# Performance work log

Hardware: AMD Instinct MI355X
Metric: run time of the kernel (lower is better)

Reference implementation:

```python
import jax, jax.numpy as jnp
import numpy as np

B, IN, HID, EMB, K = 65536, 256, 256, 64, 4096
EPS = 1e-5  # BatchNorm1d default eps


def setup_inputs() -> dict:
    key = jax.random.key(0)
    ks = jax.random.split(key, 12)
    s = 0.05
    return {
        "x": jax.random.normal(ks[0], (B, IN), jnp.float32),
        "W1": jax.random.normal(ks[1], (HID, IN), jnp.float32) * s,
        "b1": jax.random.normal(ks[2], (HID,), jnp.float32) * s,
        "gamma": jnp.ones((HID,), jnp.float32),
        "beta": jnp.zeros((HID,), jnp.float32),
        "mean": jax.random.normal(ks[3], (HID,), jnp.float32) * s,
        "var": jax.random.uniform(ks[4], (HID,), jnp.float32, 0.5, 1.5),
        "W2": jax.random.normal(ks[5], (HID // 2, HID), jnp.float32) * s,
        "b2": jax.random.normal(ks[6], (HID // 2,), jnp.float32) * s,
        "W3": jax.random.normal(ks[7], (EMB, HID // 2), jnp.float32) * s,
        "b3": jax.random.normal(ks[8], (EMB,), jnp.float32) * s,
        "codebook": jax.random.normal(ks[9], (K, EMB), jnp.float32),
    }


def reference(x, W1, b1, gamma, beta, mean, var, W2, b2, W3, b3, codebook):
    # encoder: Linear -> BatchNorm1d (eval stats) -> ReLU -> Linear -> ReLU -> Linear -> Tanh
    h = x @ W1.T + b1                                   # [B, HID]
    h = (h - mean) * jax.lax.rsqrt(var + EPS) * gamma + beta
    h = jax.nn.relu(h)
    h = jax.nn.relu(h @ W2.T + b2)                      # [B, HID//2]
    z = jnp.tanh(h @ W3.T + b3)                         # [B, EMB]
    # squared-distance matrix: ||z||^2 + ||e||^2 - 2 z e^T  -> [B, K]
    d = (jnp.sum(z * z, axis=1, keepdims=True)
         + jnp.sum(codebook * codebook, axis=1)
         - 2.0 * (z @ codebook.T))
    return jnp.argmin(d, axis=1)                        # [B] int token indices
```

## Files before the change

### kernel.cpp

```cpp
#include <hip/hip_runtime.h>

#define IN_DIM  256
#define HID_DIM 256
#define H2_DIM  128
#define EMB_DIM 64
#define K_CODES 4096
#define EPS_BN  1e-5f


typedef _Float16 f16;
typedef _Float16 f16x4 __attribute__((ext_vector_type(4)));
typedef _Float16 f16x8 __attribute__((ext_vector_type(8)));
typedef float    f32x16 __attribute__((ext_vector_type(16)));

__global__ __launch_bounds__(256) void k_norms(const float* __restrict__ cb,
                                               float* __restrict__ norms) {
    int c = blockIdx.x * 256 + threadIdx.x;
    const float4* row = reinterpret_cast<const float4*>(cb + (size_t)c * EMB_DIM);
    float s = 0.f;
#pragma unroll
    for (int i = 0; i < EMB_DIM / 4; ++i) {
        float4 v = row[i];
        s += v.x * v.x + v.y * v.y + v.z * v.z + v.w * v.w;
    }
    norms[c] = 0.5f * s;
}

__global__ __launch_bounds__(256) void k_prep(
    const float* __restrict__ W1, const float* __restrict__ W2,
    const float* __restrict__ W3, const float* __restrict__ cb,
    f16* __restrict__ p1h, f16* __restrict__ p1l,
    f16* __restrict__ p2h, f16* __restrict__ p2l,
    f16* __restrict__ p3h, f16* __restrict__ p3l,
    f16* __restrict__ cfh, f16* __restrict__ cfl) {
    int t = blockIdx.x * 256 + threadIdx.x;
    const float* src; f16 *dh, *dl; int tt, row, k0, K;
    if (t < 8192) {
        tt = t; int f = tt >> 6, l = tt & 63;
        int ct = f & 7, kst = f >> 3;
        row = ct * 32 + (l & 31); k0 = kst * 16 + (l >> 5) * 8;
        src = W1; K = IN_DIM; dh = p1h; dl = p1l;
    } else if (t < 12288) {
        tt = t - 8192; int f = tt >> 6, l = tt & 63;
        int ct = f & 3, kst = f >> 2;
        row = ct * 32 + (l & 31); k0 = kst * 16 + (l >> 5) * 8;
        src = W2; K = HID_DIM; dh = p2h; dl = p2l;
    } else if (t < 13312) {
        tt = t - 12288; int f = tt >> 6, l = tt & 63;
        int ct = f & 1, ks = f >> 1;
        row = ct * 32 + (l & 31); k0 = ks * 16 + (l >> 5) * 8;
        src = W3; K = H2_DIM; dh = p3h; dl = p3l;
    } else {
        tt = t - 13312; int f = tt >> 6, l = tt & 63;
        int ct = f & 3, ks = (f >> 2) & 3, ch = f >> 4;
        row = ch * 128 + ct * 32 + (l & 31); k0 = ks * 16 + (l >> 5) * 8;
        src = cb; K = EMB_DIM; dh = cfh; dl = cfl;
    }
    const float* s = src + (size_t)row * K + k0;
    f16x8 hv, lv;
#pragma unroll
    for (int j = 0; j < 8; ++j) {
        float v = s[j];
        f16 h = (f16)v;
        hv[j] = h;
        lv[j] = (f16)(v - (float)h);
    }
    *(f16x8*)(dh + (size_t)tt * 8) = hv;
    *(f16x8*)(dl + (size_t)tt * 8) = lv;
}

__global__ __launch_bounds__(256) void k_encoder_mfma(
    const float* __restrict__ x,
    const f16* __restrict__ p1h, const f16* __restrict__ p1l,
    const f16* __restrict__ p2h, const f16* __restrict__ p2l,
    const f16* __restrict__ p3h, const f16* __restrict__ p3l,
    const float* __restrict__ b1,
    const float* __restrict__ gm, const float* __restrict__ bt,
    const float* __restrict__ mu, const float* __restrict__ vr,
    const float* __restrict__ b2, const float* __restrict__ b3,
    f16* __restrict__ Zh, f16* __restrict__ Zl) {
    __shared__ __align__(16) f16 sm[25600];
    const int tid  = threadIdx.x;
    const int lane = tid & 63;
    const int w    = tid >> 6;
    const int ln31 = lane & 31;
    const int q    = lane >> 5;
    const int r0   = blockIdx.x * 32;

#pragma unroll
    for (int it = 0; it < 8; ++it) {
        int i = it * 256 + tid;
        int row = i >> 6, c4 = (i & 63) * 4;
        float4 v = *reinterpret_cast<const float4*>(
            x + (size_t)(r0 + row) * IN_DIM + c4);
        f16x4 hv, lv;
        hv[0] = (f16)v.x; lv[0] = (f16)(v.x - (float)hv[0]);
        hv[1] = (f16)v.y; lv[1] = (f16)(v.y - (float)hv[1]);
        hv[2] = (f16)v.z; lv[2] = (f16)(v.z - (float)hv[2]);
        hv[3] = (f16)v.w; lv[3] = (f16)(v.w - (float)hv[3]);
        *(f16x4*)(sm + row * 264 + c4)        = hv;
        *(f16x4*)(sm + 8448 + row * 264 + c4) = lv;
    }
    __syncthreads();

    f32x16 acc1a = {};
    f32x16 acc1b = {};
    {
        const f16* q1h = p1h + (size_t)(2 * w) * 512 + lane * 8;
        const f16* q1l = p1l + (size_t)(2 * w) * 512 + lane * 8;
        f16x8 bh0 = *(const f16x8*)(q1h);
        f16x8 bh1 = *(const f16x8*)(q1h + 512);
        f16x8 bl0 = *(const f16x8*)(q1l);
        f16x8 bl1 = *(const f16x8*)(q1l + 512);
#pragma unroll 2
        for (int kst = 0; kst < 16; ++kst) {
            f16x8 ch0 = bh0, ch1 = bh1, cl0 = bl0, cl1 = bl1;
            int kn = (kst + 1) & 15;
            bh0 = *(const f16x8*)(q1h + (size_t)kn * 4096);
            bh1 = *(const f16x8*)(q1h + (size_t)kn * 4096 + 512);
            bl0 = *(const f16x8*)(q1l + (size_t)kn * 4096);
            bl1 = *(const f16x8*)(q1l + (size_t)kn * 4096 + 512);
            int koff = kst * 16 + q * 8;
            f16x8 ah = *(const f16x8*)(sm + ln31 * 264 + koff);
            f16x8 al = *(const f16x8*)(sm + 8448 + ln31 * 264 + koff);
            acc1a = __builtin_amdgcn_mfma_f32_32x32x16_f16(ah, ch0, acc1a, 0, 0, 0);
            acc1b = __builtin_amdgcn_mfma_f32_32x32x16_f16(ah, ch1, acc1b, 0, 0, 0);
            acc1a = __builtin_amdgcn_mfma_f32_32x32x16_f16(al, ch0, acc1a, 0, 0, 0);
            acc1b = __builtin_amdgcn_mfma_f32_32x32x16_f16(al, ch1, acc1b, 0, 0, 0);
            acc1a = __builtin_amdgcn_mfma_f32_32x32x16_f16(ah, cl0, acc1a, 0, 0, 0);
            acc1b = __builtin_amdgcn_mfma_f32_32x32x16_f16(ah, cl1, acc1b, 0, 0, 0);
        }
    }
    __syncthreads();

    {
#pragma unroll
        for (int nt = 0; nt < 2; ++nt) {
            int j = w * 64 + nt * 32 + ln31;
            float sc = gm[j] * rsqrtf(vr[j] + EPS_BN);
            float sh = (b1[j] - mu[j]) * sc + bt[j];
            const f32x16& a = nt ? acc1b : acc1a;
#pragma unroll
            for (int r = 0; r < 16; ++r) {
                int row = (r & 3) + 8 * (r >> 2) + 4 * q;
                float v = a[r] * sc + sh;
                v = v > 0.f ? v : 0.f;
                f16 h = (f16)v;
                sm[row * 264 + j]        = h;
                sm[8448 + row * 264 + j] = (f16)(v - (float)h);
            }
        }
    }
    __syncthreads();

    f32x16 acc2a = {};
    f32x16 acc2b = {};
    {
        const f16* q2h = p2h + (size_t)w * 512 + lane * 8;
        const f16* q2l = p2l + (size_t)w * 512 + lane * 8;
        f16x8 bh = *(const f16x8*)(q2h);
        f16x8 bl = *(const f16x8*)(q2l);
#pragma unroll 2
        for (int kst = 0; kst < 16; ++kst) {
            f16x8 cbh = bh, cbl = bl;
            int kn = (kst + 1) & 15;
            bh = *(const f16x8*)(q2h + (size_t)kn * 2048);
            bl = *(const f16x8*)(q2l + (size_t)kn * 2048);
            int koff = kst * 16 + q * 8;
            f16x8 ah = *(const f16x8*)(sm + ln31 * 264 + koff);
            f16x8 al = *(const f16x8*)(sm + 8448 + ln31 * 264 + koff);
            f32x16& acc = (kst & 1) ? acc2b : acc2a;
            acc = __builtin_amdgcn_mfma_f32_32x32x16_f16(ah, cbh, acc, 0, 0, 0);
            acc = __builtin_amdgcn_mfma_f32_32x32x16_f16(al, cbh, acc, 0, 0, 0);
            acc = __builtin_amdgcn_mfma_f32_32x32x16_f16(ah, cbl, acc, 0, 0, 0);
        }
    }
    {
        int j2 = w * 32 + ln31;
        float bias = b2[j2];
#pragma unroll
        for (int r = 0; r < 16; ++r) {
            int row = (r & 3) + 8 * (r >> 2) + 4 * q;
            float v = (acc2a[r] + acc2b[r]) + bias;
            v = v > 0.f ? v : 0.f;
            f16 h = (f16)v;
            sm[16896 + row * 136 + j2] = h;
            sm[21248 + row * 136 + j2] = (f16)(v - (float)h);
        }
    }
    __syncthreads();

    if (w < 2) {
        f32x16 acc3a = {};
        f32x16 acc3b = {};
        const f16* q3h = p3h + (size_t)w * 512 + lane * 8;
        const f16* q3l = p3l + (size_t)w * 512 + lane * 8;
        f16x8 bh = *(const f16x8*)(q3h);
        f16x8 bl = *(const f16x8*)(q3l);
#pragma unroll 2
        for (int ks = 0; ks < 8; ++ks) {
            f16x8 cbh = bh, cbl = bl;
            int kn = (ks + 1) & 7;
            bh = *(const f16x8*)(q3h + (size_t)kn * 1024);
            bl = *(const f16x8*)(q3l + (size_t)kn * 1024);
            f16x8 ah = *(const f16x8*)(sm + 16896 + ln31 * 136 + ks * 16 + q * 8);
            f16x8 al = *(const f16x8*)(sm + 21248 + ln31 * 136 + ks * 16 + q * 8);
            f32x16& acc = (ks & 1) ? acc3b : acc3a;
            acc = __builtin_amdgcn_mfma_f32_32x32x16_f16(ah, cbh, acc, 0, 0, 0);
            acc = __builtin_amdgcn_mfma_f32_32x32x16_f16(al, cbh, acc, 0, 0, 0);
            acc = __builtin_amdgcn_mfma_f32_32x32x16_f16(ah, cbl, acc, 0, 0, 0);
        }
        int j3 = w * 32 + ln31;
        float bias = b3[j3];
#pragma unroll
        for (int r = 0; r < 16; ++r) {
            int row = (r & 3) + 8 * (r >> 2) + 4 * q;
            float zv = tanhf((acc3a[r] + acc3b[r]) + bias);
            f16 h = (f16)zv;
            size_t idx = (size_t)(r0 + row) * EMB_DIM + j3;
            Zh[idx] = h;
            Zl[idx] = (f16)(zv - (float)h);
        }
    }
}

__global__ __launch_bounds__(512) void k_argmin_mfma(
    const f16* __restrict__ Zh, const f16* __restrict__ Zl,
    const f16* __restrict__ cfh, const f16* __restrict__ cfl,
    const float* __restrict__ norms, int* __restrict__ out) {
    __shared__ __align__(16) f16 sm[16896];
    const int tid  = threadIdx.x;
    const int lane = tid & 63;
    const int w    = tid >> 6;
    const int rt   = w & 3;
    const int hp   = w >> 2;
    const int ln31 = lane & 31;
    const int q    = lane >> 5;
    const int r0   = blockIdx.x * 128;

    f16x8 ah[4], al[4];
#pragma unroll
    for (int ks = 0; ks < 4; ++ks) {
        size_t zoff = (size_t)(r0 + rt * 32 + ln31) * EMB_DIM + ks * 16 + q * 8;
        ah[ks] = *(const f16x8*)(Zh + zoff);
        al[ks] = *(const f16x8*)(Zl + zoff);
    }

    float bv[16];
    int   bi[16];
#pragma unroll
    for (int i = 0; i < 16; ++i) { bv[i] = -3.4e38f; bi[i] = 0; }

#pragma unroll 1
    for (int s = 0; s < 64; ++s) {
        int ch = s >> 1;
        int ct = hp * 2 + (s & 1);
        size_t fb = (size_t)(ch * 16 + ct) * 512 + lane * 8;
        f16x8 bh[4], bl[4];
#pragma unroll
        for (int ks = 0; ks < 4; ++ks) {
            bh[ks] = *(const f16x8*)(cfh + fb + (size_t)ks * 2048);
            bl[ks] = *(const f16x8*)(cfl + fb + (size_t)ks * 2048);
        }
        f32x16 acc0 = {};
        f32x16 acc1 = {};
#pragma unroll
        for (int ks = 0; ks < 4; ks += 2) {
            acc0 = __builtin_amdgcn_mfma_f32_32x32x16_f16(ah[ks],     bh[ks],     acc0, 0, 0, 0);
            acc1 = __builtin_amdgcn_mfma_f32_32x32x16_f16(ah[ks + 1], bh[ks + 1], acc1, 0, 0, 0);
            acc0 = __builtin_amdgcn_mfma_f32_32x32x16_f16(al[ks],     bh[ks],     acc0, 0, 0, 0);
            acc1 = __builtin_amdgcn_mfma_f32_32x32x16_f16(al[ks + 1], bh[ks + 1], acc1, 0, 0, 0);
            acc0 = __builtin_amdgcn_mfma_f32_32x32x16_f16(ah[ks],     bl[ks],     acc0, 0, 0, 0);
            acc1 = __builtin_amdgcn_mfma_f32_32x32x16_f16(ah[ks + 1], bl[ks + 1], acc1, 0, 0, 0);
        }
        int   col = ch * 128 + ct * 32 + ln31;
        float nv  = norms[col];
#pragma unroll
        for (int r = 0; r < 16; ++r) {
            float t  = (acc0[r] + acc1[r]) - nv;
            bool  gt = t > bv[r];
            bv[r] = gt ? t : bv[r];
            bi[r] = gt ? col : bi[r];
        }
    }

    __syncthreads();
    {
        float* pv = (float*)sm;
        int*   pi = (int*)sm + 4096;
        if (w >= 4) {
#pragma unroll
            for (int r = 0; r < 16; ++r) {
                pv[(w - 4) * 1024 + lane * 16 + r] = bv[r];
                pi[(w - 4) * 1024 + lane * 16 + r] = bi[r];
            }
        }
        __syncthreads();
        if (w < 4) {
#pragma unroll
            for (int r = 0; r < 16; ++r) {
                float v2 = pv[w * 1024 + lane * 16 + r];
                int   i2 = pi[w * 1024 + lane * 16 + r];
                bool tk = (v2 > bv[r]) || (v2 == bv[r] && i2 < bi[r]);
                bv[r] = tk ? v2 : bv[r];
                bi[r] = tk ? i2 : bi[r];
            }
        }
    }
    __syncthreads();

    float* redv = (float*)sm;
    int*   redi = (int*)sm + 4224;
    if (w < 4) {
#pragma unroll
        for (int r = 0; r < 16; ++r) {
            int row = (r & 3) + 8 * (r >> 2) + 4 * q + 32 * w;
            redv[row * 33 + ln31] = bv[r];
            redi[row * 33 + ln31] = bi[r];
        }
    }
    __syncthreads();
    if (tid < 128) {
        float v  = redv[tid * 33];
        int   ix = redi[tid * 33];
#pragma unroll
        for (int j = 1; j < 32; ++j) {
            float vj = redv[tid * 33 + j];
            int   ij = redi[tid * 33 + j];
            if (vj > v || (vj == v && ij < ix)) { v = vj; ix = ij; }
        }
        out[r0 + tid] = ix;
    }
}

extern "C" void kernel_launch(void* const* d_in, const int* in_sizes, int n_in,
                              void* d_out, int out_size, void* d_ws, size_t ws_size,
                              hipStream_t stream) {
    (void)n_in; (void)out_size; (void)ws_size;
    const float* x  = (const float*)d_in[0];
    const float* W1 = (const float*)d_in[1];
    const float* b1 = (const float*)d_in[2];
    const float* gm = (const float*)d_in[3];
    const float* bt = (const float*)d_in[4];
    const float* mu = (const float*)d_in[5];
    const float* vr = (const float*)d_in[6];
    const float* W2 = (const float*)d_in[7];
    const float* b2 = (const float*)d_in[8];
    const float* W3 = (const float*)d_in[9];
    const float* b3 = (const float*)d_in[10];
    const float* cb = (const float*)d_in[11];

    char* ws = (char*)d_ws;
    float* norms = (float*)ws;
    f16* cfh = (f16*)(ws + 16384);
    f16* cfl = (f16*)(ws + 540672);
    f16* p1h = (f16*)(ws + 1064960);
    f16* p1l = (f16*)(ws + 1196032);
    f16* p2h = (f16*)(ws + 1327104);
    f16* p2l = (f16*)(ws + 1392640);
    f16* p3h = (f16*)(ws + 1458176);
    f16* p3l = (f16*)(ws + 1474560);
    f16* Zh  = (f16*)(ws + 1490944);
    f16* Zl  = (f16*)(ws + 9879552);
    int* out = (int*)d_out;

    const int B = in_sizes[0] / IN_DIM;

    k_norms<<<K_CODES / 256, 256, 0, stream>>>(cb, norms);
    k_prep<<<180, 256, 0, stream>>>(W1, W2, W3, cb, p1h, p1l, p2h, p2l,
                                    p3h, p3l, cfh, cfl);
    k_encoder_mfma<<<B / 32, 256, 0, stream>>>(x, p1h, p1l, p2h, p2l, p3h, p3l,
                                               b1, gm, bt, mu, vr, b2, b3, Zh, Zl);
    k_argmin_mfma<<<B / 128, 512, 0, stream>>>(Zh, Zl, cfh, cfl, norms, out);
}
```

Baseline: 290.7 us.

## Split argmin codebook columns across four waves per row tile, halve rows per block

The argmin kernel now handles 64 rows per block, with 2 row tiles times 4 column-group waves instead of 4 row tiles times 2. Each wave iterates 32 chunks instead of 64, and partial results are merged through a three-step shared-memory reduction with padded strides. This doubles the block count and shortens each wave's serial loop, which improves latency hiding and load balance. In exchange, each block reuses codebook fragments across fewer rows, so codebook traffic doubles, and the merge adds extra barriers.

```diff
diff --git a/kernel.cpp b/kernel.cpp
--- a/kernel.cpp
+++ b/kernel.cpp
@@ -228,15 +228,15 @@
     const f16* __restrict__ Zh, const f16* __restrict__ Zl,
     const f16* __restrict__ cfh, const f16* __restrict__ cfl,
     const float* __restrict__ norms, int* __restrict__ out) {
-    __shared__ __align__(16) f16 sm[16896];
+    __shared__ __align__(16) float smf[4352];
     const int tid  = threadIdx.x;
     const int lane = tid & 63;
     const int w    = tid >> 6;
-    const int rt   = w & 3;
-    const int hp   = w >> 2;
+    const int rt   = w & 1;
+    const int hp   = w >> 1;
     const int ln31 = lane & 31;
     const int q    = lane >> 5;
-    const int r0   = blockIdx.x * 128;
+    const int r0   = blockIdx.x * 64;
 
     f16x8 ah[4], al[4];
 #pragma unroll
@@ -252,10 +252,8 @@
     for (int i = 0; i < 16; ++i) { bv[i] = -3.4e38f; bi[i] = 0; }
 
 #pragma unroll 1
-    for (int s = 0; s < 64; ++s) {
-        int ch = s >> 1;
-        int ct = hp * 2 + (s & 1);
-        size_t fb = (size_t)(ch * 16 + ct) * 512 + lane * 8;
+    for (int ch = 0; ch < 32; ++ch) {
+        size_t fb = (size_t)(ch * 16 + hp) * 512 + lane * 8;
         f16x8 bh[4], bl[4];
 #pragma unroll
         for (int ks = 0; ks < 4; ++ks) {
@@ -273,7 +271,7 @@
             acc0 = __builtin_amdgcn_mfma_f32_32x32x16_f16(ah[ks],     bl[ks],     acc0, 0, 0, 0);
             acc1 = __builtin_amdgcn_mfma_f32_32x32x16_f16(ah[ks + 1], bl[ks + 1], acc1, 0, 0, 0);
         }
-        int   col = ch * 128 + ct * 32 + ln31;
+        int   col = ch * 128 + hp * 32 + ln31;
         float nv  = norms[col];
 #pragma unroll
         for (int r = 0; r < 16; ++r) {
@@ -284,23 +282,24 @@
         }
     }
 
-    __syncthreads();
-    {
-        float* pv = (float*)sm;
-        int*   pi = (int*)sm + 4096;
-        if (w >= 4) {
+    float* pv = smf;
+    int*   pi = (int*)smf + 2176;
+#pragma unroll 1
+    for (int k = 1; k < 4; ++k) {
+        __syncthreads();
+        if (hp == k) {
 #pragma unroll
             for (int r = 0; r < 16; ++r) {
-                pv[(w - 4) * 1024 + lane * 16 + r] = bv[r];
-                pi[(w - 4) * 1024 + lane * 16 + r] = bi[r];
+                pv[rt * 1088 + lane * 17 + r] = bv[r];
+                pi[rt * 1088 + lane * 17 + r] = bi[r];
             }
         }
         __syncthreads();
-        if (w < 4) {
+        if (hp == 0) {
 #pragma unroll
             for (int r = 0; r < 16; ++r) {
-                float v2 = pv[w * 1024 + lane * 16 + r];
-                int   i2 = pi[w * 1024 + lane * 16 + r];
+                float v2 = pv[rt * 1088 + lane * 17 + r];
+                int   i2 = pi[rt * 1088 + lane * 17 + r];
                 bool tk = (v2 > bv[r]) || (v2 == bv[r] && i2 < bi[r]);
                 bv[r] = tk ? v2 : bv[r];
                 bi[r] = tk ? i2 : bi[r];
@@ -309,18 +308,18 @@
     }
     __syncthreads();
 
-    float* redv = (float*)sm;
-    int*   redi = (int*)sm + 4224;
-    if (w < 4) {
+    float* redv = smf;
+    int*   redi = (int*)smf + 2112;
+    if (hp == 0) {
 #pragma unroll
         for (int r = 0; r < 16; ++r) {
-            int row = (r & 3) + 8 * (r >> 2) + 4 * q + 32 * w;
+            int row = rt * 32 + (r & 3) + 8 * (r >> 2) + 4 * q;
             redv[row * 33 + ln31] = bv[r];
             redi[row * 33 + ln31] = bi[r];
         }
     }
     __syncthreads();
-    if (tid < 128) {
+    if (tid < 64) {
         float v  = redv[tid * 33];
         int   ix = redi[tid * 33];
 #pragma unroll
@@ -371,5 +370,5 @@
                                     p3h, p3l, cfh, cfl);
     k_encoder_mfma<<<B / 32, 256, 0, stream>>>(x, p1h, p1l, p2h, p2l, p3h, p3l,
                                                b1, gm, bt, mu, vr, b2, b3, Zh, Zl);
-    k_argmin_mfma<<<B / 128, 512, 0, stream>>>(Zh, Zl, cfh, cfl, norms, out);
-}
+    k_argmin_mfma<<<B / 64, 512, 0, stream>>>(Zh, Zl, cfh, cfl, norms, out);
+}
```

Result: slower. 306.6 us (+5.5%).

## Stage codebook tiles into LDS with double-buffered global_load_lds in argmin kernel

Applied to the files above, without the earlier changes.

The argmin kernel now uses 256 threads, with 4 waves each covering 32 rows across all codes, instead of 8 waves splitting the code columns in half. Each 128-code chunk of the hi/lo fp16 codebook is copied into LDS by direct global-to-LDS loads, double-buffered so the next chunk loads while the current one is consumed. This replaces per-wave global loads of codebook fragments with shared LDS reads and removes the cross-wave partial merge. In exchange it uses 64KB of LDS per block and has fewer waves per block, which may lower occupancy and latency hiding.

```diff
diff --git a/kernel.cpp b/kernel.cpp
--- a/kernel.cpp
+++ b/kernel.cpp
@@ -224,16 +224,14 @@
     }
 }
 
-__global__ __launch_bounds__(512) void k_argmin_mfma(
+__global__ __launch_bounds__(256) void k_argmin_mfma(
     const f16* __restrict__ Zh, const f16* __restrict__ Zl,
     const f16* __restrict__ cfh, const f16* __restrict__ cfl,
     const float* __restrict__ norms, int* __restrict__ out) {
-    __shared__ __align__(16) f16 sm[16896];
+    __shared__ __align__(16) f16 sm[32768];
     const int tid  = threadIdx.x;
     const int lane = tid & 63;
     const int w    = tid >> 6;
-    const int rt   = w & 3;
-    const int hp   = w >> 2;
     const int ln31 = lane & 31;
     const int q    = lane >> 5;
     const int r0   = blockIdx.x * 128;
@@ -241,7 +239,7 @@
     f16x8 ah[4], al[4];
 #pragma unroll
     for (int ks = 0; ks < 4; ++ks) {
-        size_t zoff = (size_t)(r0 + rt * 32 + ln31) * EMB_DIM + ks * 16 + q * 8;
+        size_t zoff = (size_t)(r0 + w * 32 + ln31) * EMB_DIM + ks * 16 + q * 8;
         ah[ks] = *(const f16x8*)(Zh + zoff);
         al[ks] = *(const f16x8*)(Zl + zoff);
     }
@@ -251,73 +249,75 @@
 #pragma unroll
     for (int i = 0; i < 16; ++i) { bv[i] = -3.4e38f; bi[i] = 0; }
 
+#define STAGE(CH, B) do {                                                     \
+        const f16* sH_ = cfh + (size_t)(CH) * 8192;                           \
+        const f16* sL_ = cfl + (size_t)(CH) * 8192;                           \
+        f16* dH_ = sm + (B) * 16384;                                          \
+        f16* dL_ = sm + (B) * 16384 + 8192;                                   \
+        _Pragma("unroll")                                                     \
+        for (int it_ = 0; it_ < 4; ++it_) {                                   \
+            int off_ = (it_ * 256 + tid) * 8;                                 \
+            __builtin_amdgcn_global_load_lds(                                 \
+                (const __attribute__((address_space(1))) void*)(sH_ + off_),  \
+                (__attribute__((address_space(3))) void*)(dH_ + off_),        \
+                16, 0, 0);                                                    \
+            __builtin_amdgcn_global_load_lds(                                 \
+                (const __attribute__((address_space(1))) void*)(sL_ + off_),  \
+                (__attribute__((address_space(3))) void*)(dL_ + off_),        \
+                16, 0, 0);                                                    \
+        }                                                                     \
+    } while (0)
+
+    STAGE(0, 0);
+    __syncthreads();
+
 #pragma unroll 1
-    for (int s = 0; s < 64; ++s) {
-        int ch = s >> 1;
-        int ct = hp * 2 + (s & 1);
-        size_t fb = (size_t)(ch * 16 + ct) * 512 + lane * 8;
-        f16x8 bh[4], bl[4];
-#pragma unroll
-        for (int ks = 0; ks < 4; ++ks) {
-            bh[ks] = *(const f16x8*)(cfh + fb + (size_t)ks * 2048);
-            bl[ks] = *(const f16x8*)(cfl + fb + (size_t)ks * 2048);
-        }
-        f32x16 acc0 = {};
-        f32x16 acc1 = {};
-#pragma unroll
-        for (int ks = 0; ks < 4; ks += 2) {
-            acc0 = __builtin_amdgcn_mfma_f32_32x32x16_f16(ah[ks],     bh[ks],     acc0, 0, 0, 0);
-            acc1 = __builtin_amdgcn_mfma_f32_32x32x16_f16(ah[ks + 1], bh[ks + 1], acc1, 0, 0, 0);
-            acc0 = __builtin_amdgcn_mfma_f32_32x32x16_f16(al[ks],     bh[ks],     acc0, 0, 0, 0);
-            acc1 = __builtin_amdgcn_mfma_f32_32x32x16_f16(al[ks + 1], bh[ks + 1], acc1, 0, 0, 0);
-            acc0 = __builtin_amdgcn_mfma_f32_32x32x16_f16(ah[ks],     bl[ks],     acc0, 0, 0, 0);
-            acc1 = __builtin_amdgcn_mfma_f32_32x32x16_f16(ah[ks + 1], bl[ks + 1], acc1, 0, 0, 0);
-        }
-        int   col = ch * 128 + ct * 32 + ln31;
-        float nv  = norms[col];
-#pragma unroll
-        for (int r = 0; r < 16; ++r) {
-            float t  = (acc0[r] + acc1[r]) - nv;
-            bool  gt = t > bv[r];
-            bv[r] = gt ? t : bv[r];
-            bi[r] = gt ? col : bi[r];
-        }
-    }
-
-    __syncthreads();
-    {
-        float* pv = (float*)sm;
-        int*   pi = (int*)sm + 4096;
-        if (w >= 4) {
+    for (int ch = 0; ch < 32; ++ch) {
+        int b = ch & 1;
+        if (ch + 1 < 32) STAGE(ch + 1, b ^ 1);
+        const f16* ebh = sm + b * 16384;
+        const f16* ebl = sm + b * 16384 + 8192;
+#pragma unroll 2
+        for (int ct = 0; ct < 4; ++ct) {
+            f16x8 bh[4], bl[4];
+#pragma unroll
+            for (int ks = 0; ks < 4; ++ks) {
+                int off = (ks * 4 + ct) * 512 + lane * 8;
+                bh[ks] = *(const f16x8*)(ebh + off);
+                bl[ks] = *(const f16x8*)(ebl + off);
+            }
+            f32x16 acc0 = {};
+            f32x16 acc1 = {};
+#pragma unroll
+            for (int ks = 0; ks < 4; ks += 2) {
+                acc0 = __builtin_amdgcn_mfma_f32_32x32x16_f16(ah[ks],     bh[ks],     acc0, 0, 0, 0);
+                acc1 = __builtin_amdgcn_mfma_f32_32x32x16_f16(ah[ks + 1], bh[ks + 1], acc1, 0, 0, 0);
+                acc0 = __builtin_amdgcn_mfma_f32_32x32x16_f16(al[ks],     bh[ks],     acc0, 0, 0, 0);
+                acc1 = __builtin_amdgcn_mfma_f32_32x32x16_f16(al[ks + 1], bh[ks + 1], acc1, 0, 0, 0);
+                acc0 = __builtin_amdgcn_mfma_f32_32x32x16_f16(ah[ks],     bl[ks],     acc0, 0, 0, 0);
+                acc1 = __builtin_amdgcn_mfma_f32_32x32x16_f16(ah[ks + 1], bl[ks + 1], acc1, 0, 0, 0);
+            }
+            int   col = ch * 128 + ct * 32 + ln31;
+            float nv  = norms[col];
 #pragma unroll
             for (int r = 0; r < 16; ++r) {
-                pv[(w - 4) * 1024 + lane * 16 + r] = bv[r];
-                pi[(w - 4) * 1024 + lane * 16 + r] = bi[r];
+                float t  = (acc0[r] + acc1[r]) - nv;
+                bool  gt = t > bv[r];
+                bv[r] = gt ? t : bv[r];
+                bi[r] = gt ? col : bi[r];
             }
         }
         __syncthreads();
-        if (w < 4) {
-#pragma unroll
-            for (int r = 0; r < 16; ++r) {
-                float v2 = pv[w * 1024 + lane * 16 + r];
-                int   i2 = pi[w * 1024 + lane * 16 + r];
-                bool tk = (v2 > bv[r]) || (v2 == bv[r] && i2 < bi[r]);
-                bv[r] = tk ? v2 : bv[r];
-                bi[r] = tk ? i2 : bi[r];
-            }
-        }
-    }
-    __syncthreads();
+    }
+#undef STAGE
 
     float* redv = (float*)sm;
     int*   redi = (int*)sm + 4224;
-    if (w < 4) {
-#pragma unroll
-        for (int r = 0; r < 16; ++r) {
-            int row = (r & 3) + 8 * (r >> 2) + 4 * q + 32 * w;
-            redv[row * 33 + ln31] = bv[r];
-            redi[row * 33 + ln31] = bi[r];
-        }
+#pragma unroll
+    for (int r = 0; r < 16; ++r) {
+        int row = w * 32 + (r & 3) + 8 * (r >> 2) + 4 * q;
+        redv[row * 33 + ln31] = bv[r];
+        redi[row * 33 + ln31] = bi[r];
     }
     __syncthreads();
     if (tid < 128) {
@@ -371,5 +371,5 @@
                                     p3h, p3l, cfh, cfl);
     k_encoder_mfma<<<B / 32, 256, 0, stream>>>(x, p1h, p1l, p2h, p2l, p3h, p3l,
                                                b1, gm, bt, mu, vr, b2, b3, Zh, Zl);
-    k_argmin_mfma<<<B / 128, 512, 0, stream>>>(Zh, Zl, cfh, cfl, norms, out);
-}
+    k_argmin_mfma<<<B / 128, 256, 0, stream>>>(Zh, Zl, cfh, cfl, norms, out);
+}
```

Measured after the change: 281.6 us. 1.03x faster.
